# Performance work log

Hardware: AMD Instinct MI355X
Metric: run time of the kernel (lower is better)

Reference implementation:

```python
import jax, jax.numpy as jnp
import numpy as np

WS = 4           # window_size
NUM_HEADS = 4
LN_EPS = 1e-5


def setup_inputs() -> dict:
    key = jax.random.key(0)
    ks = jax.random.split(key, 8)
    d = 256
    s = 0.02
    return {
        "feature": jax.random.normal(ks[0], (8, d, 127, 127), dtype=jnp.float32),
        "ln_w": jnp.ones((d,), jnp.float32),
        "ln_b": jnp.zeros((d,), jnp.float32),
        "in_w": jax.random.normal(ks[1], (3 * d, d), jnp.float32) * s,
        "in_b": jnp.zeros((3 * d,), jnp.float32),
        "out_w": jax.random.normal(ks[2], (d, d), jnp.float32) * s,
        "out_b": jnp.zeros((d,), jnp.float32),
        "proj_w": jax.random.normal(ks[3], (d, d), jnp.float32) * s,
        "proj_b": jnp.zeros((d,), jnp.float32),
    }


def reference(feature, ln_w, ln_b, in_w, in_b, out_w, out_b, proj_w, proj_b):
    B, C, H, W = feature.shape
    ws = WS
    pad_h = (-H) % ws
    pad_w = (-W) % ws
    x = jnp.pad(feature, ((0, 0), (0, 0), (0, pad_h), (0, pad_w)))
    Hp, Wp = H + pad_h, W + pad_w
    nh, nw = Hp // ws, Wp // ws
    # NCHW -> NHWC -> windows [B*nh*nw, ws*ws, C]
    x = x.transpose(0, 2, 3, 1)
    win = (x.reshape(B, nh, ws, nw, ws, C)
            .transpose(0, 1, 3, 2, 4, 5)
            .reshape(-1, ws * ws, C))
    # LayerNorm (ddof=0, matches torch)
    mu = win.mean(-1, keepdims=True)
    var = win.var(-1, keepdims=True)
    xn = (win - mu) / jnp.sqrt(var + LN_EPS) * ln_w + ln_b
    # fused QKV projection, then split heads
    qkv = xn @ in_w.T + in_b
    q, k, v = jnp.split(qkv, 3, axis=-1)
    hd = C // NUM_HEADS
    def heads(t):
        return t.reshape(t.shape[0], t.shape[1], NUM_HEADS, hd).transpose(0, 2, 1, 3)
    q, k, v = heads(q), heads(k), heads(v)
    scores = jnp.einsum('bhqd,bhkd->bhqk', q, k) / np.float32(np.sqrt(hd))
    a = jax.nn.softmax(scores, axis=-1)
    o = jnp.einsum('bhqk,bhkd->bhqd', a, v)
    o = o.transpose(0, 2, 1, 3).reshape(-1, ws * ws, C)
    o = o @ out_w.T + out_b
    # residual + Linear + exact GELU
    y = win + jax.nn.gelu(o @ proj_w.T + proj_b, approximate=False)
    # windows -> NHWC, crop padding, -> NCHW
    y = (y.reshape(B, nh, nw, ws, ws, C)
          .transpose(0, 1, 3, 2, 4, 5)
          .reshape(B, Hp, Wp, C))
    return y[:, :H, :W, :].transpose(0, 3, 1, 2)
```

## Files before the change

### kernel.cpp

```cpp
#include <hip/hip_runtime.h>

typedef _Float16 f16;
typedef __attribute__((ext_vector_type(4))) _Float16 half4;
typedef __attribute__((ext_vector_type(8))) _Float16 half8;
typedef __attribute__((ext_vector_type(4))) float f32x4;
typedef unsigned short u16;

#define MFMA32(a,b,c) __builtin_amdgcn_mfma_f32_16x16x32_f16(a,b,c,0,0,0)
#define MFMA16(a,b,c) __builtin_amdgcn_mfma_f32_16x16x16f16(a,b,c,0,0,0)

#define W_IN0   0
#define W_OUT0  196608
#define W_PROJ0 262144
#define X0      327680
#define QK0     33882112ull
#define VT0     100990976ull

__device__ __forceinline__ float gelu_f(float x) {
    float z = x * 0.70710678118f;
    float az = fabsf(z);
    float t = 1.f / (1.f + 0.3275911f * az);
    float e = __expf(-z * z);
    float poly = ((((1.061405429f * t - 1.453152027f) * t + 1.421413741f) * t
                   - 0.284496736f) * t + 0.254829592f) * t;
    float er = 1.f - poly * e;
    er = copysignf(er, z);
    return 0.5f * x * (1.f + er);
}

__global__ void k0_cast(const float* __restrict__ iw, const float* __restrict__ ow,
                        const float* __restrict__ pw, f16* __restrict__ W) {
    int i = blockIdx.x * 256 + threadIdx.x;
    if (i < 196608) W[W_IN0 + i] = (f16)iw[i];
    if (i < 16384) {
        const int s = i & 8191;
        const float* src = (i < 8192) ? ow : pw;
        f16* dst = W + ((i < 8192) ? W_OUT0 : W_PROJ0);
        const int g  = s & 3;
        const int r  = (s >> 2) & 31;
        const int kc = (s >> 7) & 7;
        const int ch = s >> 10;
        const int R = ch * 32 + r;
        const int c0 = kc * 32 + g * 4;
        f32x4 v0 = *(const f32x4*)(src + R * 256 + c0);
        f32x4 v1 = *(const f32x4*)(src + R * 256 + c0 + 16);
        half8 o;
#pragma unroll
        for (int j = 0; j < 4; ++j) { o[j] = (f16)v0[j]; o[j + 4] = (f16)v1[j]; }
        const int sg = g ^ ((r >> 1) & 3);
        *(half8*)(dst + ch * 8192 + kc * 1024 + r * 32 + sg * 8) = o;
    }
}

__global__ __launch_bounds__(256, 2)
void k1_pack(const float* __restrict__ feat, const float* __restrict__ lnw,
             const float* __restrict__ lnb, f16* __restrict__ X) {
    const int tid = threadIdx.x, lane = tid & 63, hh = tid >> 6;
    const int bid = blockIdx.x;
    const int jh = bid & 3, wi = (bid >> 2) & 31, bb = bid >> 7;
    const int h0 = wi * 4, w0 = jh * 32;
    const int wl4 = lane & 7, cg = lane >> 3;
    const int h = h0 + hh, wb = w0 + wl4 * 4;
    const bool hok = (h < 127);
    const bool edge = (wb + 3) >= 127;
    const size_t bbase = (size_t)bb * (256 * 127 * 127);
    const int c0 = cg * 32;
    const float* p0 = feat + bbase + (size_t)c0 * 16129 + (size_t)h * 127 + wb;

    half4 arr[32];
    float ss[4] = {0.f, 0.f, 0.f, 0.f}, qq[4] = {0.f, 0.f, 0.f, 0.f};
    if (hok && !edge) {
#pragma unroll
        for (int i = 0; i < 32; ++i) {
            f32x4 v = *(const f32x4*)(p0 + (size_t)i * 16129);
            half4 hv;
#pragma unroll
            for (int e = 0; e < 4; ++e) { ss[e] += v[e]; qq[e] += v[e] * v[e]; hv[e] = (f16)v[e]; }
            arr[i] = hv;
        }
    } else if (hok) {
#pragma unroll
        for (int i = 0; i < 32; ++i) {
            const float* pi = p0 + (size_t)i * 16129;
            half4 hv;
#pragma unroll
            for (int e = 0; e < 3; ++e) { float v = pi[e]; ss[e] += v; qq[e] += v * v; hv[e] = (f16)v; }
            hv[3] = (f16)0.f;
            arr[i] = hv;
        }
    } else {
#pragma unroll
        for (int i = 0; i < 32; ++i) {
            half4 hv; hv[0] = hv[1] = hv[2] = hv[3] = (f16)0.f; arr[i] = hv;
        }
    }
#pragma unroll
    for (int e = 0; e < 4; ++e) {
        ss[e] += __shfl_xor(ss[e], 8);  qq[e] += __shfl_xor(qq[e], 8);
        ss[e] += __shfl_xor(ss[e], 16); qq[e] += __shfl_xor(qq[e], 16);
        ss[e] += __shfl_xor(ss[e], 32); qq[e] += __shfl_xor(qq[e], 32);
    }
    float mu[4], rs[4];
#pragma unroll
    for (int e = 0; e < 4; ++e) {
        mu[e] = ss[e] * (1.f / 256.f);
        rs[e] = rsqrtf(qq[e] * (1.f / 256.f) - mu[e] * mu[e] + 1e-5f);
    }
#pragma unroll
    for (int q = 0; q < 4; ++q) {
        f32x4 lw0 = *(const f32x4*)(lnw + c0 + q * 8);
        f32x4 lw1 = *(const f32x4*)(lnw + c0 + q * 8 + 4);
        f32x4 lb0 = *(const f32x4*)(lnb + c0 + q * 8);
        f32x4 lb1 = *(const f32x4*)(lnb + c0 + q * 8 + 4);
#pragma unroll
        for (int e = 0; e < 4; ++e) {
            const int m = wl4 * 16 + hh * 4 + e;
            f16* xrow = X + ((size_t)bid * 128 + m) * 256 + c0;
            half8 o;
#pragma unroll
            for (int j = 0; j < 4; ++j) {
                o[j]     = (f16)(((float)arr[q * 8 + j][e]     - mu[e]) * rs[e] * lw0[j] + lb0[j]);
                o[j + 4] = (f16)(((float)arr[q * 8 + j + 4][e] - mu[e]) * rs[e] * lw1[j] + lb1[j]);
            }
            *(half8*)(xrow + q * 8) = o;
        }
    }
}

__global__ __launch_bounds__(512, 2)
void k2_qkv(const f16* __restrict__ X, const f16* __restrict__ win,
            const float* __restrict__ inb, f16* __restrict__ QK, f16* __restrict__ VT) {
    __shared__ __align__(16) char sm[49152];
    const int tid = threadIdx.x, lane = tid & 63, wv = tid >> 6;
    const int nwg = gridDim.x;
    const int bid = (blockIdx.x & 7) * (nwg >> 3) + (blockIdx.x >> 3);
    const int mt = bid / 6, nb = bid % 6;
    const size_t Mbase = (size_t)mt * 256;
    const int n0 = nb * 128;
    const int wm = wv >> 1, wn = wv & 1;
    const int c = lane & 15, g = lane >> 4;
    const int chs = (lane & 3) ^ ((lane >> 3) & 3);

    f32x4 acc[4][4];
#pragma unroll
    for (int a = 0; a < 4; ++a)
#pragma unroll
        for (int b = 0; b < 4; ++b) acc[a][b] = f32x4{0.f, 0.f, 0.f, 0.f};

    auto stage = [&](int step, int bsel) {
        const f16* As = X + Mbase * 256 + step * 32;
        const f16* Bs = win + (size_t)n0 * 256 + step * 32;
        char* base = sm + bsel * 24576;
#pragma unroll
        for (int p = 0; p < 2; ++p) {
            int row = p * 128 + wv * 16 + (lane >> 2);
            __builtin_amdgcn_global_load_lds(
                (const __attribute__((address_space(1))) unsigned int*)(As + (size_t)row * 256 + chs * 8),
                (__attribute__((address_space(3))) unsigned int*)(base + p * 8192 + wv * 1024),
                16, 0, 0);
        }
        {
            int row = wv * 16 + (lane >> 2);
            __builtin_amdgcn_global_load_lds(
                (const __attribute__((address_space(1))) unsigned int*)(Bs + (size_t)row * 256 + chs * 8),
                (__attribute__((address_space(3))) unsigned int*)(base + 16384 + wv * 1024),
                16, 0, 0);
        }
    };
    const int rsl = (g ^ ((c >> 1) & 3)) * 16;
    auto compute = [&](int bsel) {
        char* base = sm + bsel * 24576;
        half8 a[4], b[4];
#pragma unroll
        for (int mi = 0; mi < 4; ++mi) {
            int row = wm * 64 + mi * 16 + c;
            a[mi] = *(half8*)(base + row * 64 + rsl);
        }
#pragma unroll
        for (int nt = 0; nt < 4; ++nt) {
            int row = wn * 64 + nt * 16 + c;
            b[nt] = *(half8*)(base + 16384 + row * 64 + rsl);
        }
#pragma unroll
        for (int mi = 0; mi < 4; ++mi)
#pragma unroll
            for (int nt = 0; nt < 4; ++nt)
                acc[mi][nt] = MFMA32(a[mi], b[nt], acc[mi][nt]);
    };

    stage(0, 0);
    __syncthreads();
#pragma unroll
    for (int s = 0; s < 8; ++s) {
        const int bsel = s & 1;
        if (s < 7) stage(s + 1, bsel ^ 1);
        compute(bsel);
        __syncthreads();
    }

    const f32x4 z4 = {0.f, 0.f, 0.f, 0.f};
    half4 idf;
#pragma unroll
    for (int j = 0; j < 4; ++j) idf[j] = (f16)((g * 4 + j == c) ? 1.f : 0.f);

    if (n0 < 512) {
#pragma unroll
        for (int mi = 0; mi < 4; ++mi)
#pragma unroll
            for (int nt = 0; nt < 4; ++nt) {
                int n = n0 + wn * 64 + nt * 16 + c;
                float bias = inb[n];
                half4 h;
#pragma unroll
                for (int r = 0; r < 4; ++r) h[r] = (f16)(acc[mi][nt][r] + bias);
                f32x4 t = MFMA16(h, idf, z4);
                half4 o;
#pragma unroll
                for (int r = 0; r < 4; ++r) o[r] = (f16)t[r];
                size_t tok = Mbase + wm * 64 + mi * 16 + c;
                *(half4*)(QK + tok * 512 + (n0 + wn * 64 + nt * 16 + g * 4)) = o;
            }
    } else {
#pragma unroll
        for (int mi = 0; mi < 4; ++mi)
#pragma unroll
            for (int nt = 0; nt < 4; ++nt) {
                int n = n0 + wn * 64 + nt * 16 + c;
                float bias = inb[n];
                half4 h;
#pragma unroll
                for (int r = 0; r < 4; ++r) h[r] = (f16)(acc[mi][nt][r] + bias);
                int d = n - 512;
                size_t tokb = Mbase + wm * 64 + mi * 16;
                size_t winI = tokb >> 4;
                *(half4*)(VT + winI * 4096 + (size_t)d * 16 + g * 4) = h;
            }
    }
}

__global__ __launch_bounds__(256, 3)
void k3_attn(const f16* __restrict__ QK, const f16* __restrict__ VT,
             const f16* __restrict__ wout, const f16* __restrict__ wproj,
             const float* __restrict__ outb, const float* __restrict__ projb,
             f16* __restrict__ G) {
    __shared__ __align__(16) char sm[32768];
    const int tid = threadIdx.x, lane = tid & 63, wv = tid >> 6;
    const int c = lane & 15, g = lane >> 4;
    const size_t win = (size_t)blockIdx.x * 4 + wv;
    const f16* qrow = QK + (win * 16 + c) * 512;
    const f32x4 z4 = {0.f, 0.f, 0.f, 0.f};

    auto stageW = [&](const f16* img, int rc, int bsel) {
#pragma unroll
        for (int q2 = 0; q2 < 4; ++q2) {
            int ia = wv * 4 + q2;
            __builtin_amdgcn_global_load_lds(
                (const __attribute__((address_space(1))) unsigned int*)(img + rc * 8192 + ia * 512 + lane * 8),
                (__attribute__((address_space(3))) unsigned int*)(sm + bsel * 16384 + ia * 1024),
                16, 0, 0);
        }
    };

    stageW(wout, 0, 0);

    half8 ofp[4][2];
#pragma unroll
    for (int hq = 0; hq < 4; ++hq) {
        half8 af0 = *(const half8*)(qrow + 256 + hq * 64 + g * 8);
        half8 af1 = *(const half8*)(qrow + 256 + hq * 64 + 32 + g * 8);
        half8 bq0 = *(const half8*)(qrow + hq * 64 + g * 8);
        half8 bq1 = *(const half8*)(qrow + hq * 64 + 32 + g * 8);
        f32x4 sacc = MFMA32(af0, bq0, z4);
        sacc = MFMA32(af1, bq1, sacc);
        float s0 = sacc[0] * 0.125f, s1 = sacc[1] * 0.125f;
        float s2 = sacc[2] * 0.125f, s3 = sacc[3] * 0.125f;
        float mx = fmaxf(fmaxf(s0, s1), fmaxf(s2, s3));
        mx = fmaxf(mx, __shfl_xor(mx, 16));
        mx = fmaxf(mx, __shfl_xor(mx, 32));
        float p0 = __expf(s0 - mx), p1 = __expf(s1 - mx);
        float p2 = __expf(s2 - mx), p3 = __expf(s3 - mx);
        float sum = p0 + p1 + p2 + p3;
        sum += __shfl_xor(sum, 16);
        sum += __shfl_xor(sum, 32);
        float inv = 1.f / sum;
        half4 pf;
        pf[0] = (f16)(p0 * inv); pf[1] = (f16)(p1 * inv);
        pf[2] = (f16)(p2 * inv); pf[3] = (f16)(p3 * inv);
#pragma unroll
        for (int nt = 0; nt < 4; ++nt) {
            half4 vf = *(const half4*)(VT + win * 4096 + (size_t)(hq * 64 + nt * 16 + c) * 16 + g * 4);
            f32x4 o = MFMA16(vf, pf, z4);
#pragma unroll
            for (int r = 0; r < 4; ++r) ofp[hq][nt >> 1][(nt & 1) * 4 + r] = (f16)o[r];
        }
    }

    const int rsl = (g ^ ((c >> 1) & 3)) * 16;
    half8 obp[8];
    __syncthreads();

#pragma unroll
    for (int ch = 0; ch < 8; ++ch) {
        if (ch < 7) stageW(wout, ch + 1, (ch + 1) & 1);
        else        stageW(wproj, 0, (ch + 1) & 1);
        char* base = sm + (ch & 1) * 16384;
        f32x4 a0 = z4, a1 = z4;
#pragma unroll
        for (int kc = 0; kc < 8; ++kc) {
            half8 w0 = *(half8*)(base + kc * 2048 + c * 64 + rsl);
            a0 = MFMA32(w0, ofp[kc >> 1][kc & 1], a0);
            half8 w1 = *(half8*)(base + kc * 2048 + 1024 + c * 64 + rsl);
            a1 = MFMA32(w1, ofp[kc >> 1][kc & 1], a1);
        }
        f32x4 b0 = *(const f32x4*)(outb + ch * 32 + g * 4);
        f32x4 b1 = *(const f32x4*)(outb + ch * 32 + 16 + g * 4);
#pragma unroll
        for (int r = 0; r < 4; ++r) {
            obp[ch][r]     = (f16)(a0[r] + b0[r]);
            obp[ch][4 + r] = (f16)(a1[r] + b1[r]);
        }
        __syncthreads();
    }

#pragma unroll
    for (int pc = 0; pc < 8; ++pc) {
        if (pc < 7) stageW(wproj, pc + 1, (pc + 1) & 1);
        char* base = sm + (pc & 1) * 16384;
        f32x4 a0 = z4, a1 = z4;
#pragma unroll
        for (int kc = 0; kc < 8; ++kc) {
            half8 w0 = *(half8*)(base + kc * 2048 + c * 64 + rsl);
            a0 = MFMA32(w0, obp[kc], a0);
            half8 w1 = *(half8*)(base + kc * 2048 + 1024 + c * 64 + rsl);
            a1 = MFMA32(w1, obp[kc], a1);
        }
        f32x4 b0 = *(const f32x4*)(projb + pc * 32 + g * 4);
        f32x4 b1 = *(const f32x4*)(projb + pc * 32 + 16 + g * 4);
        half4 h0, h1;
#pragma unroll
        for (int r = 0; r < 4; ++r) {
            h0[r] = (f16)gelu_f(a0[r] + b0[r]);
            h1[r] = (f16)gelu_f(a1[r] + b1[r]);
        }
        f16* grow = G + (win * 16 + c) * 256 + pc * 32;
        *(half4*)(grow + g * 4) = h0;
        *(half4*)(grow + 16 + g * 4) = h1;
        if (pc < 7) __syncthreads();
    }
}

__global__ __launch_bounds__(256, 8)
void k4_out(const f16* __restrict__ G, const float* __restrict__ feat, float* __restrict__ outp) {
    const int tid = threadIdx.x;
    const int bid = blockIdx.x;
    const int bb = bid / 127, h = bid % 127;
    const int w = tid & 127;
    const int cq = tid >> 7;
    const bool wok = (w < 127);
    const size_t bbase = (size_t)bb * (256 * 127 * 127);
    const int wi = h >> 2, hh = h & 3;
    const int jh = w >> 5, wl4 = (w >> 2) & 7, e = w & 3;
    const size_t t = ((size_t)((bb * 32 + wi) * 4 + jh)) * 128 + wl4 * 16 + hh * 4 + e;
    const f16* gp = G + t * 256;
    const float* fp = feat + bbase + (size_t)h * 127 + w;
    float* op = outp + bbase + (size_t)h * 127 + w;
#pragma unroll 4
    for (int ci = 0; ci < 32; ++ci) {
        const int ch = ci * 8 + cq * 4;
        if (wok) {
            half4 g4 = *(const half4*)(gp + ch);
#pragma unroll
            for (int j = 0; j < 4; ++j) {
                size_t off = (size_t)(ch + j) * 16129;
                op[off] = fp[off] + (float)g4[j];
            }
        }
    }
}

extern "C" void kernel_launch(void* const* d_in, const int* in_sizes, int n_in,
                              void* d_out, int out_size, void* d_ws, size_t ws_size,
                              hipStream_t stream) {
    const float* feat   = (const float*)d_in[0];
    const float* ln_w   = (const float*)d_in[1];
    const float* ln_b   = (const float*)d_in[2];
    const float* in_w   = (const float*)d_in[3];
    const float* in_b   = (const float*)d_in[4];
    const float* out_w  = (const float*)d_in[5];
    const float* out_b  = (const float*)d_in[6];
    const float* proj_w = (const float*)d_in[7];
    const float* proj_b = (const float*)d_in[8];

    f16* W  = (f16*)d_ws;
    f16* Xb  = W + X0;
    f16* QKb = W + QK0;
    f16* VTb = W + VT0;
    f16* Gb  = Xb;

    k0_cast<<<768, 256, 0, stream>>>(in_w, out_w, proj_w, W);
    k1_pack<<<1024, 256, 0, stream>>>(feat, ln_w, ln_b, Xb);
    k2_qkv<<<3072, 512, 0, stream>>>(Xb, W + W_IN0, in_b, QKb, VTb);
    k3_attn<<<2048, 256, 0, stream>>>(QKb, VTb, W + W_OUT0, W + W_PROJ0, out_b, proj_b, Gb);
    k4_out<<<1016, 256, 0, stream>>>(Gb, feat, (float*)d_out);
}
```

Measured before the change: 367.3 us.

## Remap LayerNorm pack kernel to one image row per block with scalar coalesced loads

The pack/LayerNorm kernel now assigns one image row (all 128 width positions) per block, with each thread loading 128 channels as scalar floats and the two channel halves combined through a shared-memory reduction. This replaces the earlier mapping of 4 rows by 32 columns with float4 loads and cross-lane shuffles. The aim is fully coalesced loads along the width dimension and no misaligned vector-load edge paths, since a row stride of 127 floats leaves the old float4 loads unaligned. In exchange it issues four times as many load instructions, adds a barrier, and the output rows each thread writes are now strided 128 halves apart, reducing write contiguity.

```diff
diff --git a/kernel.cpp b/kernel.cpp
--- a/kernel.cpp
+++ b/kernel.cpp
@@ -55,75 +55,62 @@
 __global__ __launch_bounds__(256, 2)
 void k1_pack(const float* __restrict__ feat, const float* __restrict__ lnw,
              const float* __restrict__ lnb, f16* __restrict__ X) {
-    const int tid = threadIdx.x, lane = tid & 63, hh = tid >> 6;
+    __shared__ float redS[256], redQ[256];
+    const int tid = threadIdx.x;
+    const int w = tid & 127, cq = tid >> 7;
     const int bid = blockIdx.x;
-    const int jh = bid & 3, wi = (bid >> 2) & 31, bb = bid >> 7;
-    const int h0 = wi * 4, w0 = jh * 32;
-    const int wl4 = lane & 7, cg = lane >> 3;
-    const int h = h0 + hh, wb = w0 + wl4 * 4;
-    const bool hok = (h < 127);
-    const bool edge = (wb + 3) >= 127;
+    const int bb = bid >> 7, h = bid & 127;
+    const int c0 = cq * 128;
+    const bool ok = (h < 127) && (w < 127);
     const size_t bbase = (size_t)bb * (256 * 127 * 127);
-    const int c0 = cg * 32;
-    const float* p0 = feat + bbase + (size_t)c0 * 16129 + (size_t)h * 127 + wb;
-
-    half4 arr[32];
-    float ss[4] = {0.f, 0.f, 0.f, 0.f}, qq[4] = {0.f, 0.f, 0.f, 0.f};
-    if (hok && !edge) {
-#pragma unroll
-        for (int i = 0; i < 32; ++i) {
-            f32x4 v = *(const f32x4*)(p0 + (size_t)i * 16129);
-            half4 hv;
-#pragma unroll
-            for (int e = 0; e < 4; ++e) { ss[e] += v[e]; qq[e] += v[e] * v[e]; hv[e] = (f16)v[e]; }
-            arr[i] = hv;
-        }
-    } else if (hok) {
-#pragma unroll
-        for (int i = 0; i < 32; ++i) {
-            const float* pi = p0 + (size_t)i * 16129;
-            half4 hv;
-#pragma unroll
-            for (int e = 0; e < 3; ++e) { float v = pi[e]; ss[e] += v; qq[e] += v * v; hv[e] = (f16)v; }
-            hv[3] = (f16)0.f;
-            arr[i] = hv;
+    const float* p0 = feat + bbase + (size_t)c0 * 16129 + (size_t)h * 127 + w;
+
+    half8 ov[16];
+    float s = 0.f, s2 = 0.f;
+    if (ok) {
+#pragma unroll
+        for (int i = 0; i < 16; ++i) {
+            half8 hv;
+#pragma unroll
+            for (int j = 0; j < 8; ++j) {
+                float v = p0[(size_t)(i * 8 + j) * 16129];
+                s += v; s2 += v * v; hv[j] = (f16)v;
+            }
+            ov[i] = hv;
         }
     } else {
 #pragma unroll
-        for (int i = 0; i < 32; ++i) {
-            half4 hv; hv[0] = hv[1] = hv[2] = hv[3] = (f16)0.f; arr[i] = hv;
-        }
-    }
-#pragma unroll
-    for (int e = 0; e < 4; ++e) {
-        ss[e] += __shfl_xor(ss[e], 8);  qq[e] += __shfl_xor(qq[e], 8);
-        ss[e] += __shfl_xor(ss[e], 16); qq[e] += __shfl_xor(qq[e], 16);
-        ss[e] += __shfl_xor(ss[e], 32); qq[e] += __shfl_xor(qq[e], 32);
-    }
-    float mu[4], rs[4];
-#pragma unroll
-    for (int e = 0; e < 4; ++e) {
-        mu[e] = ss[e] * (1.f / 256.f);
-        rs[e] = rsqrtf(qq[e] * (1.f / 256.f) - mu[e] * mu[e] + 1e-5f);
-    }
-#pragma unroll
-    for (int q = 0; q < 4; ++q) {
-        f32x4 lw0 = *(const f32x4*)(lnw + c0 + q * 8);
-        f32x4 lw1 = *(const f32x4*)(lnw + c0 + q * 8 + 4);
-        f32x4 lb0 = *(const f32x4*)(lnb + c0 + q * 8);
-        f32x4 lb1 = *(const f32x4*)(lnb + c0 + q * 8 + 4);
-#pragma unroll
-        for (int e = 0; e < 4; ++e) {
-            const int m = wl4 * 16 + hh * 4 + e;
-            f16* xrow = X + ((size_t)bid * 128 + m) * 256 + c0;
-            half8 o;
-#pragma unroll
-            for (int j = 0; j < 4; ++j) {
-                o[j]     = (f16)(((float)arr[q * 8 + j][e]     - mu[e]) * rs[e] * lw0[j] + lb0[j]);
-                o[j + 4] = (f16)(((float)arr[q * 8 + j + 4][e] - mu[e]) * rs[e] * lw1[j] + lb1[j]);
-            }
-            *(half8*)(xrow + q * 8) = o;
-        }
+        for (int i = 0; i < 16; ++i) {
+            half8 hv;
+#pragma unroll
+            for (int j = 0; j < 8; ++j) hv[j] = (f16)0.f;
+            ov[i] = hv;
+        }
+    }
+    redS[tid] = s; redQ[tid] = s2;
+    __syncthreads();
+    float st = redS[w] + redS[w + 128];
+    float qt = redQ[w] + redQ[w + 128];
+    float mu = st * (1.f / 256.f);
+    float rs = rsqrtf(qt * (1.f / 256.f) - mu * mu + 1e-5f);
+
+    const int wi = h >> 2, hh = h & 3;
+    const int jh = w >> 5, wl4 = (w >> 2) & 7, e = w & 3;
+    const size_t t = ((size_t)((bb * 32 + wi) * 4 + jh)) * 128 + wl4 * 16 + hh * 4 + e;
+    f16* xrow = X + t * 256 + c0;
+#pragma unroll
+    for (int i = 0; i < 16; ++i) {
+        f32x4 lw0 = *(const f32x4*)(lnw + c0 + i * 8);
+        f32x4 lw1 = *(const f32x4*)(lnw + c0 + i * 8 + 4);
+        f32x4 lb0 = *(const f32x4*)(lnb + c0 + i * 8);
+        f32x4 lb1 = *(const f32x4*)(lnb + c0 + i * 8 + 4);
+        half8 o;
+#pragma unroll
+        for (int j = 0; j < 4; ++j) {
+            o[j]     = (f16)(((float)ov[i][j]     - mu) * rs * lw0[j] + lb0[j]);
+            o[j + 4] = (f16)(((float)ov[i][j + 4] - mu) * rs * lw1[j] + lb1[j]);
+        }
+        *(half8*)(xrow + i * 8) = o;
     }
 }
 
```

Result: faster. 340.3 us (-7.4%).
